# Performance work log

Hardware: AMD Instinct MI355X
Metric: run time of the kernel (lower is better)

Reference implementation:

```python
import jax, jax.numpy as jnp
import numpy as np

NUM_STEPS = 50   # global num_steps in source
SCALE = 1000     # global scale in source (fc1 out / fc2 in)
SUBTHRESH = 0.5  # HeavisideBoxcar surrogate half-width
THRESH = 1.0     # firing threshold

@jax.custom_vjp
def heaviside_boxcar(x):
    # spike = H(x); surrogate grad = boxcar of half-width SUBTHRESH
    return (x >= 0.0).astype(x.dtype)

def _hb_fwd(x):
    return heaviside_boxcar(x), x

def _hb_bwd(x, g):
    return (g * (jnp.abs(x) < SUBTHRESH).astype(g.dtype),)

heaviside_boxcar.defvjp(_hb_fwd, _hb_bwd)


def setup_inputs() -> dict:
    key = jax.random.key(0)
    k1, k2, k3 = jax.random.split(key, 3)
    B = 1024
    x = jax.random.uniform(k1, (B, 784), dtype=jnp.float32)  # pixel intensities in [0,1]
    W1 = jax.random.normal(k2, (SCALE, 784), jnp.float32) / np.sqrt(784).astype(np.float32)
    W2 = jax.random.normal(k3, (100, SCALE), jnp.float32) / np.sqrt(SCALE).astype(np.float32)
    tau_0 = jnp.array([2.0], jnp.float32)       # sigmoid(2) ~ 0.88 decay
    tau_vector = jnp.array([2.0], jnp.float32)
    acc_tau = jnp.array([2.0], jnp.float32)
    return {"x": x, "W1": W1, "W2": W2, "tau_0": tau_0,
            "tau_vector": tau_vector, "acc_tau": acc_tau}


def reference(x, W1, W2, tau_0, tau_vector, acc_tau):
    B = x.shape[0]
    # snn.spikegen.rate: per-step Bernoulli(p=x) spikes, shape [T, B, 784]
    u = jax.random.uniform(jax.random.key(42), (NUM_STEPS, B, 784), dtype=x.dtype)
    x_spk = (u < x[None]).astype(x.dtype)

    decay_0 = jax.nn.sigmoid(tau_0[0])
    decay_v = jax.nn.sigmoid(tau_vector[0])
    acc_decay = jax.nn.sigmoid(acc_tau[0])

    h1_mem = jnp.full((B, SCALE), 0.5, x.dtype)
    h1_spk = jnp.zeros((B, SCALE), x.dtype)
    h2_mem = jnp.full((B, 100), 0.5, x.dtype)
    h2_spk = jnp.zeros((B, 100), x.dtype)
    acc = jnp.zeros((B, 10), x.dtype)

    def step(carry, xt):
        h1m, h1s, h2m, h2s, acc = carry
        # pPLIF: mem = mem*decay*(1-spk) + I ; spike = H(mem - thresh)
        h1m = h1m * decay_0 * (1.0 - h1s) + xt @ W1.T
        h1s = heaviside_boxcar(h1m - THRESH)
        h2m = h2m * decay_v * (1.0 - h2s) + h1s @ W2.T
        h2s = heaviside_boxcar(h2m - THRESH)
        boost = jnp.mean(h2s.reshape(B, 10, 10), axis=2)  # AvgPool1d(10,10)
        acc = acc * acc_decay + boost                      # pPLI accumulator
        return (h1m, h1s, h2m, h2s, acc), None

    carry, _ = jax.lax.scan(step, (h1_mem, h1_spk, h2_mem, h2_spk, acc),
                            x_spk[:NUM_STEPS - 1])
    # torch loop runs under no_grad with detach(): block grads through it
    h1m, h1s, h2m, h2s, acc = jax.tree_util.tree_map(jax.lax.stop_gradient, carry)

    # final, differentiable step
    h1m = h1m * decay_0 * (1.0 - h1s) + x_spk[NUM_STEPS - 1] @ W1.T
    h1s = heaviside_boxcar(h1m - THRESH)
    h2m = h2m * decay_v * (1.0 - h2s) + h1s @ W2.T
    h2s = heaviside_boxcar(h2m - THRESH)
    boost = jnp.mean(h2s.reshape(B, 10, 10), axis=2)
    acc = acc * acc_decay + boost
    return acc
```

## Files before the change

### kernel.cpp

```cpp
#include <hip/hip_runtime.h>
#include <hip/hip_bf16.h>
#include <math.h>


#define NSTEPS 50
#define KC1 13
#define NSL 5
#define SYNC_EVERY 5

typedef __attribute__((ext_vector_type(4)))  int i32x4;
typedef __attribute__((ext_vector_type(16))) int i32x16;

#define OFF_B1     0ull
#define OFF_B2     4259840ull
#define OFF_AF     4915200ull
#define OFF_H1SC   47513600ull
#define OFF_T2     99942400ull
#define OFF_H2M    152371200ull
#define OFF_H2S    153419776ull
#define OFF_ACC    153550848ull
#define OFF_BAR    153632768ull
#define WS_END     153633280ull

#define PREP_BLOCKS 3840
#define SPK_BLOCKS 10400

__device__ __forceinline__ unsigned int rotl32(unsigned int v, int d) {
#if __has_builtin(__builtin_amdgcn_alignbit)
  return __builtin_amdgcn_alignbit(v, v, (unsigned int)(32 - d));
#else
  return (v << d) | (v >> (32 - d));
#endif
}

__device__ __forceinline__ unsigned int tf_bits(unsigned int i) {
  const unsigned int ks0 = 0u;
  const unsigned int ks1 = 42u;
  const unsigned int ks2 = 0x1BD11BDAu ^ 0u ^ 42u;
  unsigned int x0 = 0u + ks0;
  unsigned int x1 = i + ks1;
#define TF_RND(r) { x0 += x1; x1 = rotl32(x1, r); x1 ^= x0; }
  TF_RND(13) TF_RND(15) TF_RND(26) TF_RND(6)
  x0 += ks1; x1 += ks2 + 1u;
  TF_RND(17) TF_RND(29) TF_RND(16) TF_RND(24)
  x0 += ks2; x1 += ks0 + 2u;
  TF_RND(13) TF_RND(15) TF_RND(26) TF_RND(6)
  x0 += ks0; x1 += ks1 + 3u;
  TF_RND(17) TF_RND(29) TF_RND(16) TF_RND(24)
  x0 += ks1; x1 += ks2 + 4u;
  TF_RND(13) TF_RND(15) TF_RND(26) TF_RND(6)
  x0 += ks2; x1 += ks0 + 5u;
#undef TF_RND
  return x0 ^ x1;
}

__device__ __forceinline__ void spike_block(
    const float* __restrict__ x, i32x4* __restrict__ A, int gblk, int tid) {
  int g = gblk * 4 + (tid >> 6);
  int lane = tid & 63;
  int kc = g % 13;
  int r = g / 13;
  int mt = r & 63;
  int t = r >> 6;
  int b = mt * 16 + (lane & 15);
  int j0 = kc * 64 + ((lane >> 4) << 4);
  unsigned int wds[4] = {0u, 0u, 0u, 0u};
  if (j0 < 784) {
    unsigned int base = (unsigned int)(t * 1024 + b) * 784u + (unsigned int)j0;
    const float* xp = x + b * 784 + j0;
#pragma unroll
    for (int q = 0; q < 4; ++q) {
      float4 xv = *(const float4*)(xp + 4 * q);
      unsigned int K0 = (unsigned int)(int)ceilf(xv.x * 8388608.0f);
      unsigned int K1 = (unsigned int)(int)ceilf(xv.y * 8388608.0f);
      unsigned int K2 = (unsigned int)(int)ceilf(xv.z * 8388608.0f);
      unsigned int K3 = (unsigned int)(int)ceilf(xv.w * 8388608.0f);
      unsigned int w4 = 0u;
      if ((tf_bits(base + 4 * q + 0) >> 9) < K0) w4 |= 1u;
      if ((tf_bits(base + 4 * q + 1) >> 9) < K1) w4 |= 1u << 8;
      if ((tf_bits(base + 4 * q + 2) >> 9) < K2) w4 |= 1u << 16;
      if ((tf_bits(base + 4 * q + 3) >> 9) < K3) w4 |= 1u << 24;
      wds[q] = w4;
    }
  }
  i32x4 v;
  v.x = (int)wds[0]; v.y = (int)wds[1]; v.z = (int)wds[2]; v.w = (int)wds[3];
  A[(size_t)((t * 64 + mt) * 13 + kc) * 64 + lane] = v;
}

__global__ __launch_bounds__(256) void setup_kernel(
    const float* __restrict__ W1, const float* __restrict__ W2,
    signed char* __restrict__ B1, signed char* __restrict__ B2,
    const float* __restrict__ x, i32x4* __restrict__ A,
    unsigned int* __restrict__ bar) {
  if (blockIdx.x >= PREP_BLOCKS) {
    spike_block(x, A, blockIdx.x - PREP_BLOCKS, threadIdx.x);
    return;
  }
  if (blockIdx.x == 0 && threadIdx.x < 128) bar[threadIdx.x] = 0u;
  int idx = blockIdx.x * 256 + threadIdx.x;
  const int NB1 = 64 * 13 * 64 * 16;
  float w;
  signed char* dst;
  size_t stride;
  if (idx < NB1) {
    int jj = idx & 15;
    int lane = (idx >> 4) & 63;
    int kc = (idx >> 10) % 13;
    int nt = (idx >> 10) / 13;
    int k = kc * 64 + ((lane >> 4) << 4) + jj;
    int o = nt * 16 + (lane & 15);
    w = (o < 1000 && k < 784) ? W1[o * 784 + k] : 0.0f;
    dst = B1 + (size_t)(nt * 13 + kc) * 5120 + (lane << 4) + jj;
    stride = 1024;
  } else {
    int m2 = idx - NB1;
    int jj = m2 & 15;
    int lane = (m2 >> 4) & 63;
    int kc = (m2 >> 10) & 31;
    int nt = (m2 >> 10) >> 5;
    int k = kc * 32 + ((lane >> 5) << 4) + jj;
    int o = nt * 32 + (lane & 31);
    w = (o < 100 && k < 1000) ? W2[o * 1000 + k] : 0.0f;
    dst = B2 + (size_t)(nt * 32 + kc) * 1024 + (lane << 4) + jj;
    stride = 4 * 32 * 1024;
  }
  long long V = llrint((double)w * 281474976710656.0);
  signed char d = (signed char)(V & 0xFF);
  V = (V - (long long)d) >> 8;
#pragma unroll
  for (int s = 0; s < 5; ++s) {
    d = (signed char)(V & 0xFF);
    V = (V - (long long)d) >> 8;
    dst[(size_t)s * stride] = d;
  }
}

#define F1_EPI16(CP, mi, hpp, r) do {                                         \
    double td = (double)CP[4][r];                                             \
    td = td * 256.0 + (double)CP[3][r];                                       \
    td = td * 256.0 + (double)CP[2][r];                                       \
    td = td * 256.0 + (double)CP[1][r];                                       \
    td = td * 256.0 + (double)CP[0][r];                                       \
    double I = td * 0x1p-40;                                                  \
    double mm = (((spk >> (mi)) & 1u) ? 0.0 : m[mi] * alpha) + I;             \
    m[mi] = mm;                                                               \
    unsigned int sp = ((mm - 1.0) >= 0.0) ? 1u : 0u;                          \
    spk = (spk & ~(1u << (mi))) | (sp << (mi));                               \
    hpp[(r) * 16] = (signed char)sp;                                          \
  } while (0)

__global__ __launch_bounds__(512, 1) void fused1_kernel(
    const signed char* __restrict__ B1, const i32x4* __restrict__ Afc,
    signed char* __restrict__ h1sc, const float* __restrict__ tau0,
    unsigned int* __restrict__ bar) {
  extern __shared__ i32x4 blsv[];
  const int tid = threadIdx.x, lane = tid & 63, wv = tid >> 6;
  const int id = (int)blockIdx.x;
  const int mtg = id & 3, nt = id >> 2;
  const int mtA = mtg * 16 + wv * 2;
  const i32x4* B1v = (const i32x4*)B1;

  for (int r = tid; r < 2496; r += 512) {
    int kc = r / 192;
    int rem = r - kc * 192;
    blsv[r] = B1v[(size_t)nt * 4160 + (size_t)kc * 320 + rem];
  }

  i32x4 p3[13], p4[13];
#pragma unroll
  for (int kc = 0; kc < 13; ++kc) {
    p3[kc] = B1v[(size_t)nt * 4160 + (size_t)kc * 320 + 3 * 64 + lane];
    p4[kc] = B1v[(size_t)nt * 4160 + (size_t)kc * 320 + 4 * 64 + lane];
  }

  const double alpha = 1.0 / (1.0 + exp(-(double)tau0[0]));
  double m[8];
  unsigned int spk = 0;
#pragma unroll
  for (int r = 0; r < 8; ++r) m[r] = 0.5;

  i32x4 Z;
  Z.x = 0; Z.y = 0; Z.z = 0; Z.w = 0;
  i32x4 CA[5], CB[5];

  const i32x4* AtA = Afc + (size_t)(mtA * 13) * 64 + lane;
  const i32x4* AtB = AtA + 13 * 64;
  signed char* hpA = h1sc
      + ((size_t)(nt) * 1024 + mtA * 16 + ((lane >> 4) << 2)) * 16
      + (lane & 15);
  signed char* hpB = hpA + 16 * 16;

  i32x4 aA[2], aB[2];
  aA[0] = AtA[0]; aA[1] = AtA[64];
  aB[0] = AtB[0]; aB[1] = AtB[64];

  __syncthreads();

  i32x4 bR[3][3];
#pragma unroll
  for (int kc = 0; kc < 3; ++kc)
#pragma unroll
    for (int s = 0; s < 3; ++s)
      bR[kc][s] = blsv[(kc * 3 + s) * 64 + lane];

#pragma unroll 1
  for (int t = 0; t < NSTEPS; ++t) {
#pragma unroll
    for (int kc = 0; kc < 13; ++kc) {
      i32x4 avA = aA[kc & 1], avB = aB[kc & 1];
      if (kc + 2 < 13) {
        aA[kc & 1] = AtA[(kc + 2) * 64];
        aB[kc & 1] = AtB[(kc + 2) * 64];
      }
      i32x4 q0 = bR[kc % 3][0], q1 = bR[kc % 3][1], q2 = bR[kc % 3][2];
      i32x4 q3 = p3[kc], q4 = p4[kc];
      if (kc + 3 < 13) {
#pragma unroll
        for (int s = 0; s < 3; ++s)
          bR[kc % 3][s] = blsv[((kc + 3) * 3 + s) * 64 + lane];
      }
      if (kc == 0) {
        CA[0] = __builtin_amdgcn_mfma_i32_16x16x64_i8(avA, q0, Z, 0, 0, 0);
        CB[0] = __builtin_amdgcn_mfma_i32_16x16x64_i8(avB, q0, Z, 0, 0, 0);
        CA[1] = __builtin_amdgcn_mfma_i32_16x16x64_i8(avA, q1, Z, 0, 0, 0);
        CB[1] = __builtin_amdgcn_mfma_i32_16x16x64_i8(avB, q1, Z, 0, 0, 0);
        CA[2] = __builtin_amdgcn_mfma_i32_16x16x64_i8(avA, q2, Z, 0, 0, 0);
        CB[2] = __builtin_amdgcn_mfma_i32_16x16x64_i8(avB, q2, Z, 0, 0, 0);
        CA[3] = __builtin_amdgcn_mfma_i32_16x16x64_i8(avA, q3, Z, 0, 0, 0);
        CB[3] = __builtin_amdgcn_mfma_i32_16x16x64_i8(avB, q3, Z, 0, 0, 0);
        CA[4] = __builtin_amdgcn_mfma_i32_16x16x64_i8(avA, q4, Z, 0, 0, 0);
        CB[4] = __builtin_amdgcn_mfma_i32_16x16x64_i8(avB, q4, Z, 0, 0, 0);
      } else {
        CA[0] = __builtin_amdgcn_mfma_i32_16x16x64_i8(avA, q0, CA[0], 0, 0, 0);
        CB[0] = __builtin_amdgcn_mfma_i32_16x16x64_i8(avB, q0, CB[0], 0, 0, 0);
        CA[1] = __builtin_amdgcn_mfma_i32_16x16x64_i8(avA, q1, CA[1], 0, 0, 0);
        CB[1] = __builtin_amdgcn_mfma_i32_16x16x64_i8(avB, q1, CB[1], 0, 0, 0);
        CA[2] = __builtin_amdgcn_mfma_i32_16x16x64_i8(avA, q2, CA[2], 0, 0, 0);
        CB[2] = __builtin_amdgcn_mfma_i32_16x16x64_i8(avB, q2, CB[2], 0, 0, 0);
        CA[3] = __builtin_amdgcn_mfma_i32_16x16x64_i8(avA, q3, CA[3], 0, 0, 0);
        CB[3] = __builtin_amdgcn_mfma_i32_16x16x64_i8(avB, q3, CB[3], 0, 0, 0);
        CA[4] = __builtin_amdgcn_mfma_i32_16x16x64_i8(avA, q4, CA[4], 0, 0, 0);
        CB[4] = __builtin_amdgcn_mfma_i32_16x16x64_i8(avB, q4, CB[4], 0, 0, 0);
      }
    }
    if (t + 1 < NSTEPS) { AtA += 53248; AtB += 53248; }
    aA[0] = AtA[0]; aA[1] = AtA[64];
    aB[0] = AtB[0]; aB[1] = AtB[64];
#pragma unroll
    for (int kc = 0; kc < 3; ++kc)
#pragma unroll
      for (int s = 0; s < 3; ++s)
        bR[kc][s] = blsv[(kc * 3 + s) * 64 + lane];
#pragma unroll
    for (int r = 0; r < 4; ++r) F1_EPI16(CA, r, hpA, r);
#pragma unroll
    for (int r = 0; r < 4; ++r) F1_EPI16(CB, r + 4, hpB, r);
    hpA += 1048576; hpB += 1048576;
    if (((t + 1) % SYNC_EVERY) == 0 && (t + 1) < NSTEPS) {
      __syncthreads();
      if (tid == 0) {
        int ph = (t + 1) / SYNC_EVERY - 1;
        unsigned int* c = bar + (mtg << 4) + ph;
        __hip_atomic_fetch_add(c, 1u, __ATOMIC_RELAXED,
                               __HIP_MEMORY_SCOPE_AGENT);
        for (int spin = 0; spin < 20000; ++spin) {
          if (__hip_atomic_load(c, __ATOMIC_RELAXED,
                                __HIP_MEMORY_SCOPE_AGENT) >= 64u) break;
          __builtin_amdgcn_s_sleep(2);
        }
      }
      __syncthreads();
    }
  }
}

__global__ __launch_bounds__(256, 3) void gemm2_kernel(
    const signed char* __restrict__ Bf, const signed char* __restrict__ h1sc,
    double* __restrict__ T2) {
  __shared__ i32x4 bls[2][NSL][64];
  int tid = threadIdx.x, lane = tid & 63, wv = tid >> 6;
  int nt = blockIdx.x & 3;
  int mg = blockIdx.x >> 2;
  int tl = mg >> 3;
  int mt = ((mg & 7) << 2) + wv;
  const i32x4* Ar = (const i32x4*)h1sc
      + ((size_t)tl * 64 + (lane >> 5)) * 1024 + mt * 32 + (lane & 31);
  const i32x4* Bp = (const i32x4*)Bf + lane;
  const bool st4 = (wv == 0);
#define B2_IDX(s, kc) ((size_t)(((s) * 4 + nt) * 32 + (kc)) * 64)

  i32x16 C[NSL];
#pragma unroll
  for (int s = 0; s < NSL; ++s)
#pragma unroll
    for (int i = 0; i < 16; ++i) C[s][i] = 0;

  i32x4 sa = Bp[B2_IDX(wv, 0)];
  i32x4 sb; if (st4) sb = Bp[B2_IDX(4, 0)];
  i32x4 a0 = Ar[0];
  i32x4 a1 = Ar[2048];
  i32x4 a2;
  bls[0][wv][lane] = sa;
  if (st4) bls[0][4][lane] = sb;
  sa = Bp[B2_IDX(wv, 1)];
  if (st4) sb = Bp[B2_IDX(4, 1)];
  __syncthreads();

  for (int kc = 0; kc < 32; ++kc) {
    const int cur = kc & 1, nxt = cur ^ 1;
    if (kc + 1 < 32) {
      bls[nxt][wv][lane] = sa;
      if (st4) bls[nxt][4][lane] = sb;
    }
    if (kc + 2 < 32) {
      sa = Bp[B2_IDX(wv, kc + 2)];
      if (st4) sb = Bp[B2_IDX(4, kc + 2)];
      a2 = Ar[(size_t)(kc + 2) * 2048];
    }
    i32x4 b0 = bls[cur][0][lane], b1 = bls[cur][1][lane], b2 = bls[cur][2][lane];
    i32x4 b3 = bls[cur][3][lane], b4 = bls[cur][4][lane];
    C[0] = __builtin_amdgcn_mfma_i32_32x32x32_i8(a0, b0, C[0], 0, 0, 0);
    C[1] = __builtin_amdgcn_mfma_i32_32x32x32_i8(a0, b1, C[1], 0, 0, 0);
    C[2] = __builtin_amdgcn_mfma_i32_32x32x32_i8(a0, b2, C[2], 0, 0, 0);
    C[3] = __builtin_amdgcn_mfma_i32_32x32x32_i8(a0, b3, C[3], 0, 0, 0);
    C[4] = __builtin_amdgcn_mfma_i32_32x32x32_i8(a0, b4, C[4], 0, 0, 0);
    a0 = a1; a1 = a2;
    __syncthreads();
  }

  int o = nt * 32 + (lane & 31);
  int rb = 4 * (lane >> 5);
#pragma unroll
  for (int r = 0; r < 16; ++r) {
    int row = (r & 3) + 8 * (r >> 2) + rb;
    int b = mt * 32 + row;
    long long T = (long long)C[4][r];
    T = (T << 8) + (long long)C[3][r];
    T = (T << 8) + (long long)C[2][r];
    T = (T << 8) + (long long)C[1][r];
    T = (T << 8) + (long long)C[0][r];
    T2[((size_t)tl * 1024 + b) * 128 + o] = (double)T * 0x1p-40;
  }
}

__global__ __launch_bounds__(256) void rec2_kernel(
    const double* __restrict__ T2, double* __restrict__ h2m_st,
    signed char* __restrict__ h2s_st, double* __restrict__ acc_st,
    const float* __restrict__ tauv, const float* __restrict__ acct,
    int t0, int C, float* __restrict__ out) {
  __shared__ signed char sp[256];
  int tid = threadIdx.x;
  int b = blockIdx.x * 2 + (tid >> 7);
  int o = tid & 127;
  double alpha = 1.0 / (1.0 + exp(-(double)tauv[0]));
  double adec  = 1.0 / (1.0 + exp(-(double)acct[0]));
  double m, s, accv = 0.0;
  bool isPool = (o < 10);
  if (t0 == 0) {
    m = 0.5; s = 0.0;
  } else {
    m = h2m_st[(size_t)b * 128 + o];
    s = (double)h2s_st[(size_t)b * 128 + o];
    if (isPool) accv = acc_st[b * 10 + o];
  }
  for (int tl = 0; tl < C; ++tl) {
    double I = T2[((size_t)tl * 1024 + b) * 128 + o];
    m = (s != 0.0 ? 0.0 : m * alpha) + I;
    bool spk = (m - 1.0) >= 0.0;
    s = spk ? 1.0 : 0.0;
    sp[tid] = spk ? 1 : 0;
    __syncthreads();
    if (isPool) {
      int base = tid & 128;
      int isum = 0;
#pragma unroll
      for (int k = 0; k < 10; ++k) isum += sp[base + o * 10 + k];
      accv = accv * adec + (double)isum / 10.0;
      if (t0 + tl == NSTEPS - 1) out[b * 10 + o] = (float)accv;
    }
    __syncthreads();
  }
  h2m_st[(size_t)b * 128 + o] = m;
  h2s_st[(size_t)b * 128 + o] = (signed char)(s != 0.0 ? 1 : 0);
  if (isPool) acc_st[b * 10 + o] = accv;
}

extern "C" void kernel_launch(void* const* d_in, const int* in_sizes, int n_in,
                              void* d_out, int out_size, void* d_ws, size_t ws_size,
                              hipStream_t stream) {
  const float* x    = (const float*)d_in[0];
  const float* W1   = (const float*)d_in[1];
  const float* W2   = (const float*)d_in[2];
  const float* tau0 = (const float*)d_in[3];
  const float* tauv = (const float*)d_in[4];
  const float* acct = (const float*)d_in[5];
  float* out = (float*)d_out;
  char*  ws  = (char*)d_ws;

  signed char* B1     = (signed char*)(ws + OFF_B1);
  signed char* B2     = (signed char*)(ws + OFF_B2);
  signed char* Af     = (signed char*)(ws + OFF_AF);
  signed char* h1sc   = (signed char*)(ws + OFF_H1SC);
  double*      T2     = (double*)(ws + OFF_T2);
  double*      h2m_st = (double*)(ws + OFF_H2M);
  signed char* h2s_st = (signed char*)(ws + OFF_H2S);
  double*      acc_st = (double*)(ws + OFF_ACC);
  unsigned int* bar   = (unsigned int*)(ws + OFF_BAR);
  i32x4*       Afv    = (i32x4*)Af;

  static bool attr_done = false;
  if (!attr_done) {
    (void)hipFuncSetAttribute((const void*)fused1_kernel,
                              hipFuncAttributeMaxDynamicSharedMemorySize,
                              39936);
    attr_done = true;
  }

  setup_kernel<<<PREP_BLOCKS + SPK_BLOCKS, 256, 0, stream>>>(
      W1, W2, B1, B2, x, Afv, bar);

  fused1_kernel<<<256, 512, 39936, stream>>>(B1, Afv, h1sc, tau0, bar);

  gemm2_kernel<<<4 * NSTEPS * 8, 256, 0, stream>>>(B2, h1sc, T2);

  rec2_kernel<<<512, 256, 0, stream>>>(
      T2, h2m_st, h2s_st, acc_st, tauv, acct, 0, NSTEPS, out);
}
```

Before: 464.6 us.

## Software-pipeline fused1 timesteps, overlapping epilogue with next step's MFMAs

Restructures the fused1 time loop with two sets of accumulators, so the membrane/spike epilogue of step t is interleaved with the MFMA chain of step t+1. The A-fragment prefetch now crosses step boundaries. It also moves B-slice 3 from registers into LDS, growing dynamic shared memory to 53248 bytes, and switches to a 2-deep 4-wide register buffer for B. The aim is to hide epilogue latency and the per-step load bubble, at the cost of more accumulator registers and more LDS traffic.

```diff
diff --git a/kernel.cpp b/kernel.cpp
--- a/kernel.cpp
+++ b/kernel.cpp
@@ -150,6 +150,60 @@
     hpp[(r) * 16] = (signed char)sp;                                          \
   } while (0)
 
+#define F1_STEP(WA, WB, EA, EB, DOEPI, LAST, PAR) do {                        \
+    _Pragma("unroll")                                                         \
+    for (int kc = 0; kc < 13; ++kc) {                                         \
+      const int sl = (kc + (PAR)) & 1;                                        \
+      i32x4 avA = aA[sl], avB = aB[sl];                                       \
+      if (kc + 2 < 13) {                                                      \
+        aA[sl] = AtA[(kc + 2) * 64];                                          \
+        aB[sl] = AtB[(kc + 2) * 64];                                          \
+      } else if (!(LAST)) {                                                   \
+        aA[sl] = AtA[(kc + 2 - 13) * 64 + 53248];                             \
+        aB[sl] = AtB[(kc + 2 - 13) * 64 + 53248];                             \
+      }                                                                       \
+      i32x4 q0 = bR[sl][0], q1 = bR[sl][1],                                   \
+            q2 = bR[sl][2], q3 = bR[sl][3];                                   \
+      i32x4 q4 = p4[kc];                                                      \
+      if (kc + 2 < 13) {                                                      \
+        _Pragma("unroll")                                                     \
+        for (int s = 0; s < 4; ++s)                                           \
+          bR[sl][s] = blsv[((kc + 2) * 4 + s) * 64 + lane];                   \
+      } else {                                                                \
+        _Pragma("unroll")                                                     \
+        for (int s = 0; s < 4; ++s)                                           \
+          bR[sl][s] = blsv[((kc + 2 - 13) * 4 + s) * 64 + lane];              \
+      }                                                                       \
+      if (kc == 0) {                                                          \
+        WA[0] = __builtin_amdgcn_mfma_i32_16x16x64_i8(avA, q0, Z, 0, 0, 0);   \
+        WB[0] = __builtin_amdgcn_mfma_i32_16x16x64_i8(avB, q0, Z, 0, 0, 0);   \
+        WA[1] = __builtin_amdgcn_mfma_i32_16x16x64_i8(avA, q1, Z, 0, 0, 0);   \
+        WB[1] = __builtin_amdgcn_mfma_i32_16x16x64_i8(avB, q1, Z, 0, 0, 0);   \
+        WA[2] = __builtin_amdgcn_mfma_i32_16x16x64_i8(avA, q2, Z, 0, 0, 0);   \
+        WB[2] = __builtin_amdgcn_mfma_i32_16x16x64_i8(avB, q2, Z, 0, 0, 0);   \
+        WA[3] = __builtin_amdgcn_mfma_i32_16x16x64_i8(avA, q3, Z, 0, 0, 0);   \
+        WB[3] = __builtin_amdgcn_mfma_i32_16x16x64_i8(avB, q3, Z, 0, 0, 0);   \
+        WA[4] = __builtin_amdgcn_mfma_i32_16x16x64_i8(avA, q4, Z, 0, 0, 0);   \
+        WB[4] = __builtin_amdgcn_mfma_i32_16x16x64_i8(avB, q4, Z, 0, 0, 0);   \
+      } else {                                                                \
+        WA[0] = __builtin_amdgcn_mfma_i32_16x16x64_i8(avA, q0, WA[0], 0,0,0); \
+        WB[0] = __builtin_amdgcn_mfma_i32_16x16x64_i8(avB, q0, WB[0], 0,0,0); \
+        WA[1] = __builtin_amdgcn_mfma_i32_16x16x64_i8(avA, q1, WA[1], 0,0,0); \
+        WB[1] = __builtin_amdgcn_mfma_i32_16x16x64_i8(avB, q1, WB[1], 0,0,0); \
+        WA[2] = __builtin_amdgcn_mfma_i32_16x16x64_i8(avA, q2, WA[2], 0,0,0); \
+        WB[2] = __builtin_amdgcn_mfma_i32_16x16x64_i8(avB, q2, WB[2], 0,0,0); \
+        WA[3] = __builtin_amdgcn_mfma_i32_16x16x64_i8(avA, q3, WA[3], 0,0,0); \
+        WB[3] = __builtin_amdgcn_mfma_i32_16x16x64_i8(avB, q3, WB[3], 0,0,0); \
+        WA[4] = __builtin_amdgcn_mfma_i32_16x16x64_i8(avA, q4, WA[4], 0,0,0); \
+        WB[4] = __builtin_amdgcn_mfma_i32_16x16x64_i8(avB, q4, WB[4], 0,0,0); \
+      }                                                                       \
+      if ((DOEPI) && kc >= 1 && kc <= 4) F1_EPI16(EA, kc - 1, hpA, kc - 1);   \
+      if ((DOEPI) && kc >= 5 && kc <= 8) F1_EPI16(EB, kc - 1, hpB, kc - 5);   \
+    }                                                                         \
+    if (DOEPI) { hpA += 1048576; hpB += 1048576; }                            \
+    if (!(LAST)) { AtA += 53248; AtB += 53248; }                              \
+  } while (0)
+
 __global__ __launch_bounds__(512, 1) void fused1_kernel(
     const signed char* __restrict__ B1, const i32x4* __restrict__ Afc,
     signed char* __restrict__ h1sc, const float* __restrict__ tau0,
@@ -161,18 +215,16 @@
   const int mtA = mtg * 16 + wv * 2;
   const i32x4* B1v = (const i32x4*)B1;
 
-  for (int r = tid; r < 2496; r += 512) {
-    int kc = r / 192;
-    int rem = r - kc * 192;
+  for (int r = tid; r < 3328; r += 512) {
+    int kc = r >> 8;
+    int rem = r & 255;
     blsv[r] = B1v[(size_t)nt * 4160 + (size_t)kc * 320 + rem];
   }
 
-  i32x4 p3[13], p4[13];
-#pragma unroll
-  for (int kc = 0; kc < 13; ++kc) {
-    p3[kc] = B1v[(size_t)nt * 4160 + (size_t)kc * 320 + 3 * 64 + lane];
+  i32x4 p4[13];
+#pragma unroll
+  for (int kc = 0; kc < 13; ++kc)
     p4[kc] = B1v[(size_t)nt * 4160 + (size_t)kc * 320 + 4 * 64 + lane];
-  }
 
   const double alpha = 1.0 / (1.0 + exp(-(double)tau0[0]));
   double m[8];
@@ -182,7 +234,8 @@
 
   i32x4 Z;
   Z.x = 0; Z.y = 0; Z.z = 0; Z.w = 0;
-  i32x4 CA[5], CB[5];
+  i32x4 Ca[5], Cb[5];
+  i32x4 Da[5], Db[5];
 
   const i32x4* AtA = Afc + (size_t)(mtA * 13) * 64 + lane;
   const i32x4* AtB = AtA + 13 * 64;
@@ -197,70 +250,22 @@
 
   __syncthreads();
 
-  i32x4 bR[3][3];
-#pragma unroll
-  for (int kc = 0; kc < 3; ++kc)
-#pragma unroll
-    for (int s = 0; s < 3; ++s)
-      bR[kc][s] = blsv[(kc * 3 + s) * 64 + lane];
-
+  i32x4 bR[2][4];
+#pragma unroll
+  for (int kc = 0; kc < 2; ++kc)
+#pragma unroll
+    for (int s = 0; s < 4; ++s)
+      bR[kc][s] = blsv[(kc * 4 + s) * 64 + lane];
+
+  F1_STEP(Ca, Cb, Da, Db, 0, 0, 0);
 #pragma unroll 1
-  for (int t = 0; t < NSTEPS; ++t) {
-#pragma unroll
-    for (int kc = 0; kc < 13; ++kc) {
-      i32x4 avA = aA[kc & 1], avB = aB[kc & 1];
-      if (kc + 2 < 13) {
-        aA[kc & 1] = AtA[(kc + 2) * 64];
-        aB[kc & 1] = AtB[(kc + 2) * 64];
-      }
-      i32x4 q0 = bR[kc % 3][0], q1 = bR[kc % 3][1], q2 = bR[kc % 3][2];
-      i32x4 q3 = p3[kc], q4 = p4[kc];
-      if (kc + 3 < 13) {
-#pragma unroll
-        for (int s = 0; s < 3; ++s)
-          bR[kc % 3][s] = blsv[((kc + 3) * 3 + s) * 64 + lane];
-      }
-      if (kc == 0) {
-        CA[0] = __builtin_amdgcn_mfma_i32_16x16x64_i8(avA, q0, Z, 0, 0, 0);
-        CB[0] = __builtin_amdgcn_mfma_i32_16x16x64_i8(avB, q0, Z, 0, 0, 0);
-        CA[1] = __builtin_amdgcn_mfma_i32_16x16x64_i8(avA, q1, Z, 0, 0, 0);
-        CB[1] = __builtin_amdgcn_mfma_i32_16x16x64_i8(avB, q1, Z, 0, 0, 0);
-        CA[2] = __builtin_amdgcn_mfma_i32_16x16x64_i8(avA, q2, Z, 0, 0, 0);
-        CB[2] = __builtin_amdgcn_mfma_i32_16x16x64_i8(avB, q2, Z, 0, 0, 0);
-        CA[3] = __builtin_amdgcn_mfma_i32_16x16x64_i8(avA, q3, Z, 0, 0, 0);
-        CB[3] = __builtin_amdgcn_mfma_i32_16x16x64_i8(avB, q3, Z, 0, 0, 0);
-        CA[4] = __builtin_amdgcn_mfma_i32_16x16x64_i8(avA, q4, Z, 0, 0, 0);
-        CB[4] = __builtin_amdgcn_mfma_i32_16x16x64_i8(avB, q4, Z, 0, 0, 0);
-      } else {
-        CA[0] = __builtin_amdgcn_mfma_i32_16x16x64_i8(avA, q0, CA[0], 0, 0, 0);
-        CB[0] = __builtin_amdgcn_mfma_i32_16x16x64_i8(avB, q0, CB[0], 0, 0, 0);
-        CA[1] = __builtin_amdgcn_mfma_i32_16x16x64_i8(avA, q1, CA[1], 0, 0, 0);
-        CB[1] = __builtin_amdgcn_mfma_i32_16x16x64_i8(avB, q1, CB[1], 0, 0, 0);
-        CA[2] = __builtin_amdgcn_mfma_i32_16x16x64_i8(avA, q2, CA[2], 0, 0, 0);
-        CB[2] = __builtin_amdgcn_mfma_i32_16x16x64_i8(avB, q2, CB[2], 0, 0, 0);
-        CA[3] = __builtin_amdgcn_mfma_i32_16x16x64_i8(avA, q3, CA[3], 0, 0, 0);
-        CB[3] = __builtin_amdgcn_mfma_i32_16x16x64_i8(avB, q3, CB[3], 0, 0, 0);
-        CA[4] = __builtin_amdgcn_mfma_i32_16x16x64_i8(avA, q4, CA[4], 0, 0, 0);
-        CB[4] = __builtin_amdgcn_mfma_i32_16x16x64_i8(avB, q4, CB[4], 0, 0, 0);
-      }
-    }
-    if (t + 1 < NSTEPS) { AtA += 53248; AtB += 53248; }
-    aA[0] = AtA[0]; aA[1] = AtA[64];
-    aB[0] = AtB[0]; aB[1] = AtB[64];
-#pragma unroll
-    for (int kc = 0; kc < 3; ++kc)
-#pragma unroll
-      for (int s = 0; s < 3; ++s)
-        bR[kc][s] = blsv[(kc * 3 + s) * 64 + lane];
-#pragma unroll
-    for (int r = 0; r < 4; ++r) F1_EPI16(CA, r, hpA, r);
-#pragma unroll
-    for (int r = 0; r < 4; ++r) F1_EPI16(CB, r + 4, hpB, r);
-    hpA += 1048576; hpB += 1048576;
-    if (((t + 1) % SYNC_EVERY) == 0 && (t + 1) < NSTEPS) {
+  for (int tp = 0; tp < 24; ++tp) {
+    F1_STEP(Da, Db, Ca, Cb, 1, 0, 1);
+    F1_STEP(Ca, Cb, Da, Db, 1, 0, 0);
+    if (((tp + 1) % 5) == 0) {
       __syncthreads();
       if (tid == 0) {
-        int ph = (t + 1) / SYNC_EVERY - 1;
+        int ph = (tp + 1) / 5 - 1;
         unsigned int* c = bar + (mtg << 4) + ph;
         __hip_atomic_fetch_add(c, 1u, __ATOMIC_RELAXED,
                                __HIP_MEMORY_SCOPE_AGENT);
@@ -273,6 +278,11 @@
       __syncthreads();
     }
   }
+  F1_STEP(Da, Db, Ca, Cb, 1, 1, 1);
+#pragma unroll
+  for (int r = 0; r < 4; ++r) F1_EPI16(Da, r, hpA, r);
+#pragma unroll
+  for (int r = 0; r < 4; ++r) F1_EPI16(Db, r + 4, hpB, r);
 }
 
 __global__ __launch_bounds__(256, 3) void gemm2_kernel(
@@ -413,14 +423,14 @@
   if (!attr_done) {
     (void)hipFuncSetAttribute((const void*)fused1_kernel,
                               hipFuncAttributeMaxDynamicSharedMemorySize,
-                              39936);
+                              53248);
     attr_done = true;
   }
 
   setup_kernel<<<PREP_BLOCKS + SPK_BLOCKS, 256, 0, stream>>>(
       W1, W2, B1, B2, x, Afv, bar);
 
-  fused1_kernel<<<256, 512, 39936, stream>>>(B1, Afv, h1sc, tau0, bar);
+  fused1_kernel<<<256, 512, 53248, stream>>>(B1, Afv, h1sc, tau0, bar);
 
   gemm2_kernel<<<4 * NSTEPS * 8, 256, 0, stream>>>(B2, h1sc, T2);
 
```

Measured after the change: 406.3 us. 1.14x faster.
